# Kernel tuning notes

Hardware: AMD Instinct MI355X
Metric: run time of the kernel (lower is better)

## Reference

```python
import jax, jax.numpy as jnp
import numpy as np

B, S, D = 32, 576, 768
G = 24  # sqrt(S)
TEMP = 0.01


def grid_sample_bilinear_zeros(img, grid):
    # img: (B,C,H,W), grid: (B,Hg,Wg,2) in [-1,1]; torch F.grid_sample,
    # mode='bilinear', padding_mode='zeros', align_corners=False
    Bn, C, H, W = img.shape
    gx, gy = grid[..., 0], grid[..., 1]
    ix = ((gx + 1.0) * W - 1.0) * 0.5
    iy = ((gy + 1.0) * H - 1.0) * 0.5
    x0 = jnp.floor(ix); y0 = jnp.floor(iy)
    x1 = x0 + 1.0;      y1 = y0 + 1.0
    wx1 = ix - x0; wx0 = 1.0 - wx1
    wy1 = iy - y0; wy0 = 1.0 - wy1

    def gather(xi, yi):
        valid = (xi >= 0) & (xi <= W - 1) & (yi >= 0) & (yi <= H - 1)
        xc = jnp.clip(xi, 0, W - 1).astype(jnp.int32)
        yc = jnp.clip(yi, 0, H - 1).astype(jnp.int32)
        vals = jax.vmap(lambda im, y, x: im[:, y, x])(img, yc, xc)  # (B,C,Hg,Wg)
        return vals * valid.astype(img.dtype)[:, None, :, :]

    return (gather(x0, y0) * (wx0 * wy0)[:, None]
            + gather(x1, y0) * (wx1 * wy0)[:, None]
            + gather(x0, y1) * (wx0 * wy1)[:, None]
            + gather(x1, y1) * (wx1 * wy1)[:, None])


def key_finder_net(h, W1, b1, W2, b2, W3, b3):
    # fc1 -> relu -> fc2 -> relu -> fc3 -> tanh
    h = jax.nn.relu(h @ W1 + b1)
    h = jax.nn.relu(h @ W2 + b2)
    return jnp.tanh(h @ W3 + b3)


def setup_inputs() -> dict:
    key = jax.random.key(0)
    ks = jax.random.split(key, 16)
    sd = 1.0 / np.sqrt(D)
    inp = {
        'x': jax.random.normal(ks[0], (B, S, D), dtype=jnp.float32),
        'indices': jax.random.randint(ks[1], (B, S), 0, S),
        'Wq': jax.random.normal(ks[2], (D, D), dtype=jnp.float32) * sd,
        'bq': jnp.zeros((D,), jnp.float32),
        'Wk': jax.random.normal(ks[3], (D, D), dtype=jnp.float32) * sd,
        'bk': jnp.zeros((D,), jnp.float32),
        'Wv': jax.random.normal(ks[4], (D, D), dtype=jnp.float32) * sd,
        'bv': jnp.zeros((D,), jnp.float32),
        'W1': jax.random.normal(ks[5], (2 * D, 60), dtype=jnp.float32) / np.sqrt(2 * D),
        'b1': jnp.zeros((60,), jnp.float32),
        'W2': jax.random.normal(ks[6], (60, 60), dtype=jnp.float32) / np.sqrt(60),
        'b2': jnp.zeros((60,), jnp.float32),
        'W3': jax.random.normal(ks[7], (60, 2), dtype=jnp.float32) / np.sqrt(60),
        'b3': jnp.zeros((2,), jnp.float32),
    }
    return inp


def reference(x, indices, Wq, bq, Wk, bk, Wv, bv, W1, b1, W2, b2, W3, b3):
    q = x @ Wq + bq  # (B,S,D)
    k = x @ Wk + bk
    v = x @ Wv + bv

    sample = key_finder_net(jnp.concatenate([q, k], axis=2), W1, b1, W2, b2, W3, b3)  # (B,S,2)
    # torch: cat((sample_x, sample_y), dim=1).reshape(B,G,G,2)
    flat = jnp.concatenate([sample[:, :, 0], sample[:, :, 1]], axis=1)  # (B,2S)
    grid = flat.reshape(B, G, G, 2)

    k_img = jnp.transpose(k, (0, 2, 1)).reshape(B, D, G, G)
    v_img = jnp.transpose(v, (0, 2, 1)).reshape(B, D, G, G)

    sk = grid_sample_bilinear_zeros(k_img, grid)  # (B,D,G,G)
    sv = grid_sample_bilinear_zeros(v_img, grid)
    sampled_key = jnp.transpose(sk.reshape(B, D, G * G), (0, 2, 1))   # (B,S,D)
    sampled_value = jnp.transpose(sv.reshape(B, D, G * G), (0, 2, 1))

    scores = jnp.sum(q * sampled_key, axis=-1)  # (B,S)
    return jax.nn.sigmoid(TEMP * scores)[..., None] * sampled_value
```

## Files before the change

kernel.cpp:

```cpp
#include <hip/hip_runtime.h>

typedef _Float16 f16;
typedef _Float16 f16x8 __attribute__((ext_vector_type(8)));
typedef _Float16 f16x4 __attribute__((ext_vector_type(4)));
typedef float f32x4 __attribute__((ext_vector_type(4)));

constexpr int NB = 32, NS = 576, ND = 768, NG = 24;
constexpr int M_TOT = NB * NS;
constexpr int N_TOT = 3 * ND;

__global__ void cast_x_kernel(const float* __restrict__ x, f16* __restrict__ xb) {
  int i = (blockIdx.x * 256 + threadIdx.x) * 4;
  float4 v = *(const float4*)(x + i);
  f16x4 o;
  o.x = (f16)v.x; o.y = (f16)v.y; o.z = (f16)v.z; o.w = (f16)v.w;
  *(f16x4*)(xb + i) = o;
}

__global__ void cast_w_kernel(const float* __restrict__ Wq, const float* __restrict__ Wk,
                              const float* __restrict__ Wv, f16* __restrict__ WT) {
  int t = blockIdx.x * 256 + threadIdx.x;
  int n = t / ND, k = t % ND;
  const float* src = (n >= 2 * ND) ? Wv : ((n >= ND) ? Wk : Wq);
  int nn = (n >= 2 * ND) ? n - 2 * ND : ((n >= ND) ? n - ND : n);
  WT[t] = (f16)src[k * ND + nn];
}

__global__ void wcT_kernel(const float* __restrict__ Wq, const float* __restrict__ Wk,
                           const float* __restrict__ bq, const float* __restrict__ bk,
                           const float* __restrict__ W1, const float* __restrict__ b1,
                           f16* __restrict__ WcT_hi, f16* __restrict__ WcT_lo,
                           float* __restrict__ bc) {
  if (blockIdx.x == 192) {
    int c = threadIdx.x;
    if (c < 60) {
      float acc = b1[c];
      for (int j = 0; j < ND; j++)
        acc += bq[j] * W1[j * 60 + c] + bk[j] * W1[(ND + j) * 60 + c];
      bc[c] = acc;
    }
    return;
  }
  int flat = blockIdx.x * 256 + threadIdx.x;
  int r = flat >> 6, c = flat & 63;
  float acc = 0.f;
  if (c < 60) {
    const float* wq = Wq + (size_t)r * ND;
    const float* wk = Wk + (size_t)r * ND;
    for (int j = 0; j < ND; j++)
      acc += wq[j] * W1[j * 60 + c] + wk[j] * W1[(ND + j) * 60 + c];
  }
  f16 hi = (f16)acc;
  f16 lo = (f16)(acc - (float)hi);
  WcT_hi[(size_t)c * ND + r] = hi;
  WcT_lo[(size_t)c * ND + r] = lo;
}

__device__ __forceinline__ void async_copy16(const f16* g, f16* l) {
  __builtin_amdgcn_global_load_lds((const __attribute__((address_space(1))) void*)g,
                                   (__attribute__((address_space(3))) void*)l, 16, 0, 0);
}

__global__ __launch_bounds__(256) void gemm_kernel(const f16* __restrict__ A,
                                                   const f16* __restrict__ Bt,
                                                   const float* __restrict__ bq,
                                                   const float* __restrict__ bk,
                                                   const float* __restrict__ bv,
                                                   f16* __restrict__ C) {
  constexpr int BM = 128, BN = 128, BK = 32;
  __shared__ __align__(16) f16 sA[BM * BK];
  __shared__ __align__(16) f16 sB[BN * BK];

  int bm = blockIdx.x % (M_TOT / BM);
  int bn = blockIdx.x / (M_TOT / BM);
  int tid = threadIdx.x;
  int wave = tid >> 6, lane = tid & 63;
  int wm = (wave >> 1) * 64, wn = (wave & 1) * 64;
  int m0 = bm * BM, n0 = bn * BN;

  int srow = tid >> 2;
  int skc = (tid & 3) * 8;

  f32x4 acc[4][4];
#pragma unroll
  for (int i = 0; i < 4; i++)
#pragma unroll
    for (int j = 0; j < 4; j++) acc[i][j] = 0.f;

  int q = lane >> 4, r16 = lane & 15;

  for (int kk = 0; kk < ND; kk += BK) {
    async_copy16(A + (size_t)(m0 + srow) * ND + kk + skc, sA + tid * 8);
    async_copy16(A + (size_t)(m0 + 64 + srow) * ND + kk + skc, sA + 2048 + tid * 8);
    async_copy16(Bt + (size_t)(n0 + srow) * ND + kk + skc, sB + tid * 8);
    async_copy16(Bt + (size_t)(n0 + 64 + srow) * ND + kk + skc, sB + 2048 + tid * 8);
    __syncthreads();

    f16x8 aF[4], bF[4];
#pragma unroll
    for (int mt = 0; mt < 4; mt++)
      aF[mt] = *(const f16x8*)(sA + (wm + mt * 16 + r16) * BK + q * 8);
#pragma unroll
    for (int nt = 0; nt < 4; nt++)
      bF[nt] = *(const f16x8*)(sB + (wn + nt * 16 + r16) * BK + q * 8);
#pragma unroll
    for (int mt = 0; mt < 4; mt++)
#pragma unroll
      for (int nt = 0; nt < 4; nt++)
        acc[mt][nt] = __builtin_amdgcn_mfma_f32_16x16x32_f16(aF[mt], bF[nt], acc[mt][nt], 0, 0, 0);
    __syncthreads();
  }

#pragma unroll
  for (int nt = 0; nt < 4; nt++) {
    int gn = n0 + wn + nt * 16 + r16;
    float bias = (gn < ND) ? bq[gn] : ((gn < 2 * ND) ? bk[gn - ND] : bv[gn - 2 * ND]);
#pragma unroll
    for (int mt = 0; mt < 4; mt++) {
#pragma unroll
      for (int r = 0; r < 4; r++) {
        int gm = m0 + wm + mt * 16 + q * 4 + r;
        C[(size_t)gm * N_TOT + gn] = (f16)(acc[mt][nt][r] + bias);
      }
    }
  }
}

__global__ __launch_bounds__(256) void z1_mfma_kernel(const float* __restrict__ x,
                                                      const f16* __restrict__ WcT_hi,
                                                      const f16* __restrict__ WcT_lo,
                                                      const float* __restrict__ bc,
                                                      float* __restrict__ h1) {
  int wave = threadIdx.x >> 6, lane = threadIdx.x & 63;
  int q = lane >> 4, r16 = lane & 15;
  int m0 = blockIdx.x * 64 + wave * 16;
  const float* xr = x + (size_t)(m0 + r16) * ND;

  f32x4 acc[4];
#pragma unroll
  for (int nf = 0; nf < 4; nf++) acc[nf] = 0.f;

  for (int kk = 0; kk < ND; kk += 32) {
    int ko = kk + q * 8;
    float4 v0 = *(const float4*)(xr + ko);
    float4 v1 = *(const float4*)(xr + ko + 4);
    f16x8 a_hi, a_lo;
    float xv[8] = {v0.x, v0.y, v0.z, v0.w, v1.x, v1.y, v1.z, v1.w};
#pragma unroll
    for (int j = 0; j < 8; j++) {
      f16 h = (f16)xv[j];
      a_hi[j] = h;
      a_lo[j] = (f16)(xv[j] - (float)h);
    }
    f16x8 b_hi[4], b_lo[4];
#pragma unroll
    for (int nf = 0; nf < 4; nf++) {
      size_t off = (size_t)(nf * 16 + r16) * ND + ko;
      b_hi[nf] = *(const f16x8*)(WcT_hi + off);
      b_lo[nf] = *(const f16x8*)(WcT_lo + off);
    }
#pragma unroll
    for (int nf = 0; nf < 4; nf++) {
      acc[nf] = __builtin_amdgcn_mfma_f32_16x16x32_f16(a_hi, b_hi[nf], acc[nf], 0, 0, 0);
      acc[nf] = __builtin_amdgcn_mfma_f32_16x16x32_f16(a_lo, b_hi[nf], acc[nf], 0, 0, 0);
      acc[nf] = __builtin_amdgcn_mfma_f32_16x16x32_f16(a_hi, b_lo[nf], acc[nf], 0, 0, 0);
    }
  }

#pragma unroll
  for (int nf = 0; nf < 4; nf++) {
    int col = nf * 16 + r16;
    if (col < 60) {
      float bcv = bc[col];
#pragma unroll
      for (int r = 0; r < 4; r++)
        h1[(size_t)(m0 + q * 4 + r) * 60 + col] = fmaxf(acc[nf][r] + bcv, 0.f);
    }
  }
}

__global__ void mlp_tail_kernel(const float* __restrict__ h1, const float* __restrict__ W2,
                                const float* __restrict__ b2, const float* __restrict__ W3,
                                const float* __restrict__ b3, float* __restrict__ coords) {
  int m = (blockIdx.x * 256 + threadIdx.x) >> 6;
  int lane = threadIdx.x & 63;
  int cl = (lane < 60) ? lane : 59;
  const float* h = h1 + (size_t)m * 60;
  float acc = b2[cl];
  for (int j = 0; j < 60; j++) acc = fmaf(h[j], W2[j * 60 + cl], acc);
  float h2 = fmaxf(acc, 0.f);
  float p0 = (lane < 60) ? h2 * W3[cl * 2 + 0] : 0.f;
  float p1 = (lane < 60) ? h2 * W3[cl * 2 + 1] : 0.f;
#pragma unroll
  for (int o = 32; o > 0; o >>= 1) { p0 += __shfl_down(p0, o); p1 += __shfl_down(p1, o); }
  if (lane == 0) {
    float s0 = tanhf(p0 + b3[0]);
    float s1 = tanhf(p1 + b3[1]);
    int b = m / NS, s = m % NS;
    float* cb = coords + (size_t)b * (2 * NS);
    cb[(s >> 1) * 2 + (s & 1)] = s0;
    cb[(288 + (s >> 1)) * 2 + (s & 1)] = s1;
  }
}

__global__ __launch_bounds__(256) void sample_kernel(const f16* __restrict__ qkv,
                                                     const float* __restrict__ coords,
                                                     float* __restrict__ out) {
  int blk = blockIdx.x;
  int b = blk / NS, p = blk % NS;
  int tid = threadIdx.x;

  float gx = coords[(size_t)b * (2 * NS) + p * 2 + 0];
  float gy = coords[(size_t)b * (2 * NS) + p * 2 + 1];
  float ix = ((gx + 1.f) * (float)NG - 1.f) * 0.5f;
  float iy = ((gy + 1.f) * (float)NG - 1.f) * 0.5f;
  float x0f = floorf(ix), y0f = floorf(iy);
  float wx1 = ix - x0f, wx0 = 1.f - wx1;
  float wy1 = iy - y0f, wy0 = 1.f - wy1;
  int x0 = (int)x0f, y0 = (int)y0f, x1 = x0 + 1, y1 = y0 + 1;
  bool vx0 = (x0 >= 0) & (x0 <= NG - 1), vx1 = (x1 >= 0) & (x1 <= NG - 1);
  bool vy0 = (y0 >= 0) & (y0 <= NG - 1), vy1 = (y1 >= 0) & (y1 <= NG - 1);
  int cx0 = min(max(x0, 0), NG - 1), cx1 = min(max(x1, 0), NG - 1);
  int cy0 = min(max(y0, 0), NG - 1), cy1 = min(max(y1, 0), NG - 1);
  float w00 = wx0 * wy0 * ((vx0 && vy0) ? 1.f : 0.f);
  float w10 = wx1 * wy0 * ((vx1 && vy0) ? 1.f : 0.f);
  float w01 = wx0 * wy1 * ((vx0 && vy1) ? 1.f : 0.f);
  float w11 = wx1 * wy1 * ((vx1 && vy1) ? 1.f : 0.f);

  size_t base = (size_t)b * NS;
  const f16* r00 = qkv + (base + cy0 * NG + cx0) * N_TOT;
  const f16* r10 = qkv + (base + cy0 * NG + cx1) * N_TOT;
  const f16* r01 = qkv + (base + cy1 * NG + cx0) * N_TOT;
  const f16* r11 = qkv + (base + cy1 * NG + cx1) * N_TOT;
  const f16* qr  = qkv + (base + p) * N_TOT;

  float partial = 0.f;
  float svs[3];
#pragma unroll
  for (int i = 0; i < 3; i++) {
    int d = tid + i * 256;
    float sk = w00 * (float)r00[ND + d] + w10 * (float)r10[ND + d]
             + w01 * (float)r01[ND + d] + w11 * (float)r11[ND + d];
    float sv = w00 * (float)r00[2 * ND + d] + w10 * (float)r10[2 * ND + d]
             + w01 * (float)r01[2 * ND + d] + w11 * (float)r11[2 * ND + d];
    partial = fmaf((float)qr[d], sk, partial);
    svs[i] = sv;
  }
  __shared__ float red[4];
#pragma unroll
  for (int o = 32; o > 0; o >>= 1) partial += __shfl_down(partial, o);
  if ((tid & 63) == 0) red[tid >> 6] = partial;
  __syncthreads();
  float score = red[0] + red[1] + red[2] + red[3];
  float sig = 1.f / (1.f + expf(-0.01f * score));
  float* orow = out + (size_t)(base + p) * ND;
#pragma unroll
  for (int i = 0; i < 3; i++) orow[tid + i * 256] = sig * svs[i];
}

extern "C" void kernel_launch(void* const* d_in, const int* in_sizes, int n_in,
                              void* d_out, int out_size, void* d_ws, size_t ws_size,
                              hipStream_t stream) {
  const float* x  = (const float*)d_in[0];
  const float* Wq = (const float*)d_in[2];
  const float* bq = (const float*)d_in[3];
  const float* Wk = (const float*)d_in[4];
  const float* bk = (const float*)d_in[5];
  const float* Wv = (const float*)d_in[6];
  const float* bv = (const float*)d_in[7];
  const float* W1 = (const float*)d_in[8];
  const float* b1 = (const float*)d_in[9];
  const float* W2 = (const float*)d_in[10];
  const float* b2 = (const float*)d_in[11];
  const float* W3 = (const float*)d_in[12];
  const float* b3 = (const float*)d_in[13];
  float* out = (float*)d_out;

  char* ws = (char*)d_ws;
  f16*   xb     = (f16*)(ws);
  f16*   WT     = (f16*)(ws + 28311552);
  f16*   qkv    = (f16*)(ws + 31850496);
  f16*   WcT_hi = (f16*)(ws);
  f16*   WcT_lo = (f16*)(ws + 98304);
  float* bc     = (float*)(ws + 116969472);
  float* h1     = (float*)(ws + 116969728);
  float* coords = (float*)(ws + 121393408);

  cast_x_kernel<<<dim3(M_TOT * ND / 1024), dim3(256), 0, stream>>>(x, xb);
  cast_w_kernel<<<dim3(N_TOT * ND / 256), dim3(256), 0, stream>>>(Wq, Wk, Wv, WT);
  gemm_kernel<<<dim3((M_TOT / 128) * (N_TOT / 128)), dim3(256), 0, stream>>>(xb, WT, bq, bk, bv, qkv);
  wcT_kernel<<<dim3(193), dim3(256), 0, stream>>>(Wq, Wk, bq, bk, W1, b1, WcT_hi, WcT_lo, bc);
  z1_mfma_kernel<<<dim3(M_TOT / 64), dim3(256), 0, stream>>>(x, WcT_hi, WcT_lo, bc, h1);
  mlp_tail_kernel<<<dim3(M_TOT / 4), dim3(256), 0, stream>>>(h1, W2, b2, W3, b3, coords);
  sample_kernel<<<dim3(M_TOT), dim3(256), 0, stream>>>(qkv, coords, out);
  (void)in_sizes; (void)n_in; (void)out_size; (void)ws_size;
}
```

Baseline: 411.3 us.

## Fuse x cast into z1, transpose W via LDS, split Wc reduction, vectorize sampler

The standalone x-to-f16 cast is removed; the z1 kernel now writes the f16 high part of x as a side output for the QKV GEMM, so x is read from HBM once. The weight cast-transpose goes through a 64x64 shared-memory tile so both reads and writes are coalesced. The Wq/Wk·W1 precompute is split along K across 8× more blocks with atomic accumulation into a zeroed fp32 buffer, followed by a separate hi/lo split pass. The sampler uses one wave per output row with f16x4 loads and float4 stores, so no LDS reduction or barrier is needed. The trade-offs are extra launches and a memset, plus atomic accumulation order that is not deterministic.

New measurement: 417.7 us. Within noise of the previous version (+1.6%).

```diff
diff --git a/kernel.cpp b/kernel.cpp
--- a/kernel.cpp
+++ b/kernel.cpp
@@ -9,28 +9,50 @@
 constexpr int M_TOT = NB * NS;
 constexpr int N_TOT = 3 * ND;
 
-__global__ void cast_x_kernel(const float* __restrict__ x, f16* __restrict__ xb) {
-  int i = (blockIdx.x * 256 + threadIdx.x) * 4;
-  float4 v = *(const float4*)(x + i);
-  f16x4 o;
-  o.x = (f16)v.x; o.y = (f16)v.y; o.z = (f16)v.z; o.w = (f16)v.w;
-  *(f16x4*)(xb + i) = o;
-}
-
-__global__ void cast_w_kernel(const float* __restrict__ Wq, const float* __restrict__ Wk,
-                              const float* __restrict__ Wv, f16* __restrict__ WT) {
-  int t = blockIdx.x * 256 + threadIdx.x;
-  int n = t / ND, k = t % ND;
-  const float* src = (n >= 2 * ND) ? Wv : ((n >= ND) ? Wk : Wq);
-  int nn = (n >= 2 * ND) ? n - 2 * ND : ((n >= ND) ? n - ND : n);
-  WT[t] = (f16)src[k * ND + nn];
-}
-
-__global__ void wcT_kernel(const float* __restrict__ Wq, const float* __restrict__ Wk,
-                           const float* __restrict__ bq, const float* __restrict__ bk,
-                           const float* __restrict__ W1, const float* __restrict__ b1,
-                           f16* __restrict__ WcT_hi, f16* __restrict__ WcT_lo,
-                           float* __restrict__ bc) {
+__global__ __launch_bounds__(256) void cast_w_t_kernel(const float* __restrict__ Wq,
+                                                       const float* __restrict__ Wk,
+                                                       const float* __restrict__ Wv,
+                                                       f16* __restrict__ WT) {
+  __shared__ float tile[64][65];
+  int bt = blockIdx.x;
+  int ntile = bt / 12, ktile = bt % 12;
+  const float* src = (ntile < 12) ? Wq : ((ntile < 24) ? Wk : Wv);
+  int n0 = (ntile % 12) * 64, k0 = ktile * 64;
+  int cc = threadIdx.x & 63, rr = threadIdx.x >> 6;
+#pragma unroll
+  for (int i = 0; i < 16; i++) {
+    int k = rr + i * 4;
+    tile[cc][k] = src[(size_t)(k0 + k) * ND + n0 + cc];
+  }
+  __syncthreads();
+#pragma unroll
+  for (int i = 0; i < 16; i++) {
+    int n = rr + i * 4;
+    WT[(size_t)(ntile * 64 + n) * ND + k0 + cc] = (f16)tile[n][cc];
+  }
+}
+
+__global__ void wc_partial_kernel(const float* __restrict__ Wq, const float* __restrict__ Wk,
+                                  const float* __restrict__ W1, float* __restrict__ WcfT) {
+  int b = blockIdx.x;
+  int rb = b % 192, jc = b / 192;
+  int flat = rb * 256 + threadIdx.x;
+  int r = flat >> 6, c = flat & 63;
+  if (c >= 60) return;
+  const float* wq = Wq + (size_t)r * ND;
+  const float* wk = Wk + (size_t)r * ND;
+  float acc = 0.f;
+  int j0 = jc * 96;
+  for (int j = j0; j < j0 + 96; j++)
+    acc += wq[j] * W1[j * 60 + c] + wk[j] * W1[(ND + j) * 60 + c];
+  atomicAdd(&WcfT[(size_t)c * ND + r], acc);
+}
+
+__global__ void wc_split_kernel(const float* __restrict__ WcfT,
+                                const float* __restrict__ bq, const float* __restrict__ bk,
+                                const float* __restrict__ W1, const float* __restrict__ b1,
+                                f16* __restrict__ WcT_hi, f16* __restrict__ WcT_lo,
+                                float* __restrict__ bc) {
   if (blockIdx.x == 192) {
     int c = threadIdx.x;
     if (c < 60) {
@@ -41,19 +63,11 @@
     }
     return;
   }
-  int flat = blockIdx.x * 256 + threadIdx.x;
-  int r = flat >> 6, c = flat & 63;
-  float acc = 0.f;
-  if (c < 60) {
-    const float* wq = Wq + (size_t)r * ND;
-    const float* wk = Wk + (size_t)r * ND;
-    for (int j = 0; j < ND; j++)
-      acc += wq[j] * W1[j * 60 + c] + wk[j] * W1[(ND + j) * 60 + c];
-  }
-  f16 hi = (f16)acc;
-  f16 lo = (f16)(acc - (float)hi);
-  WcT_hi[(size_t)c * ND + r] = hi;
-  WcT_lo[(size_t)c * ND + r] = lo;
+  int t = blockIdx.x * 256 + threadIdx.x;
+  float v = WcfT[t];
+  f16 h = (f16)v;
+  WcT_hi[t] = h;
+  WcT_lo[t] = (f16)(v - (float)h);
 }
 
 __device__ __forceinline__ void async_copy16(const f16* g, f16* l) {
@@ -67,16 +81,16 @@
                                                    const float* __restrict__ bk,
                                                    const float* __restrict__ bv,
                                                    f16* __restrict__ C) {
-  constexpr int BM = 128, BN = 128, BK = 32;
+  constexpr int BM = 128, BK = 32;
   __shared__ __align__(16) f16 sA[BM * BK];
-  __shared__ __align__(16) f16 sB[BN * BK];
+  __shared__ __align__(16) f16 sB[BM * BK];
 
   int bm = blockIdx.x % (M_TOT / BM);
   int bn = blockIdx.x / (M_TOT / BM);
   int tid = threadIdx.x;
   int wave = tid >> 6, lane = tid & 63;
   int wm = (wave >> 1) * 64, wn = (wave & 1) * 64;
-  int m0 = bm * BM, n0 = bn * BN;
+  int m0 = bm * BM, n0 = bn * BM;
 
   int srow = tid >> 2;
   int skc = (tid & 3) * 8;
@@ -130,7 +144,8 @@
                                                       const f16* __restrict__ WcT_hi,
                                                       const f16* __restrict__ WcT_lo,
                                                       const float* __restrict__ bc,
-                                                      float* __restrict__ h1) {
+                                                      float* __restrict__ h1,
+                                                      f16* __restrict__ xb) {
   int wave = threadIdx.x >> 6, lane = threadIdx.x & 63;
   int q = lane >> 4, r16 = lane & 15;
   int m0 = blockIdx.x * 64 + wave * 16;
@@ -152,6 +167,7 @@
       a_hi[j] = h;
       a_lo[j] = (f16)(xv[j] - (float)h);
     }
+    *(f16x8*)(xb + (size_t)(m0 + r16) * ND + ko) = a_hi;
     f16x8 b_hi[4], b_lo[4];
 #pragma unroll
     for (int nf = 0; nf < 4; nf++) {
@@ -203,12 +219,12 @@
   }
 }
 
-__global__ __launch_bounds__(256) void sample_kernel(const f16* __restrict__ qkv,
-                                                     const float* __restrict__ coords,
-                                                     float* __restrict__ out) {
+__global__ __launch_bounds__(64) void sample_kernel(const f16* __restrict__ qkv,
+                                                    const float* __restrict__ coords,
+                                                    float* __restrict__ out) {
   int blk = blockIdx.x;
   int b = blk / NS, p = blk % NS;
-  int tid = threadIdx.x;
+  int t = threadIdx.x;
 
   float gx = coords[(size_t)b * (2 * NS) + p * 2 + 0];
   float gy = coords[(size_t)b * (2 * NS) + p * 2 + 1];
@@ -234,28 +250,43 @@
   const f16* r11 = qkv + (base + cy1 * NG + cx1) * N_TOT;
   const f16* qr  = qkv + (base + p) * N_TOT;
 
+  int d0 = t * 12;
   float partial = 0.f;
-  float svs[3];
-#pragma unroll
-  for (int i = 0; i < 3; i++) {
-    int d = tid + i * 256;
-    float sk = w00 * (float)r00[ND + d] + w10 * (float)r10[ND + d]
-             + w01 * (float)r01[ND + d] + w11 * (float)r11[ND + d];
-    float sv = w00 * (float)r00[2 * ND + d] + w10 * (float)r10[2 * ND + d]
-             + w01 * (float)r01[2 * ND + d] + w11 * (float)r11[2 * ND + d];
-    partial = fmaf((float)qr[d], sk, partial);
-    svs[i] = sv;
-  }
-  __shared__ float red[4];
+  float outv[12];
+#pragma unroll
+  for (int ch = 0; ch < 3; ch++) {
+    int d = d0 + ch * 4;
+    f16x4 k00 = *(const f16x4*)(r00 + ND + d);
+    f16x4 k10 = *(const f16x4*)(r10 + ND + d);
+    f16x4 k01 = *(const f16x4*)(r01 + ND + d);
+    f16x4 k11 = *(const f16x4*)(r11 + ND + d);
+    f16x4 v00 = *(const f16x4*)(r00 + 2 * ND + d);
+    f16x4 v10 = *(const f16x4*)(r10 + 2 * ND + d);
+    f16x4 v01 = *(const f16x4*)(r01 + 2 * ND + d);
+    f16x4 v11 = *(const f16x4*)(r11 + 2 * ND + d);
+    f16x4 qv  = *(const f16x4*)(qr + d);
+#pragma unroll
+    for (int j = 0; j < 4; j++) {
+      float sk = w00 * (float)k00[j] + w10 * (float)k10[j]
+               + w01 * (float)k01[j] + w11 * (float)k11[j];
+      float sv = w00 * (float)v00[j] + w10 * (float)v10[j]
+               + w01 * (float)v01[j] + w11 * (float)v11[j];
+      partial = fmaf((float)qv[j], sk, partial);
+      outv[ch * 4 + j] = sv;
+    }
+  }
 #pragma unroll
   for (int o = 32; o > 0; o >>= 1) partial += __shfl_down(partial, o);
-  if ((tid & 63) == 0) red[tid >> 6] = partial;
-  __syncthreads();
-  float score = red[0] + red[1] + red[2] + red[3];
+  float score = __shfl(partial, 0);
   float sig = 1.f / (1.f + expf(-0.01f * score));
   float* orow = out + (size_t)(base + p) * ND;
 #pragma unroll
-  for (int i = 0; i < 3; i++) orow[tid + i * 256] = sig * svs[i];
+  for (int ch = 0; ch < 3; ch++) {
+    float4 st;
+    st.x = sig * outv[ch * 4 + 0]; st.y = sig * outv[ch * 4 + 1];
+    st.z = sig * outv[ch * 4 + 2]; st.w = sig * outv[ch * 4 + 3];
+    *(float4*)(orow + d0 + ch * 4) = st;
+  }
 }
 
 extern "C" void kernel_launch(void* const* d_in, const int* in_sizes, int n_in,
@@ -280,18 +311,20 @@
   f16*   xb     = (f16*)(ws);
   f16*   WT     = (f16*)(ws + 28311552);
   f16*   qkv    = (f16*)(ws + 31850496);
-  f16*   WcT_hi = (f16*)(ws);
-  f16*   WcT_lo = (f16*)(ws + 98304);
+  f16*   WcT_hi = (f16*)(ws + 31850496);
+  f16*   WcT_lo = (f16*)(ws + 31948800);
+  float* WcfT   = (float*)(ws + 32047104);
   float* bc     = (float*)(ws + 116969472);
   float* h1     = (float*)(ws + 116969728);
   float* coords = (float*)(ws + 121393408);
 
-  cast_x_kernel<<<dim3(M_TOT * ND / 1024), dim3(256), 0, stream>>>(x, xb);
-  cast_w_kernel<<<dim3(N_TOT * ND / 256), dim3(256), 0, stream>>>(Wq, Wk, Wv, WT);
+  cast_w_t_kernel<<<dim3(432), dim3(256), 0, stream>>>(Wq, Wk, Wv, WT);
+  hipMemsetAsync(WcfT, 0, 64 * ND * sizeof(float), stream);
+  wc_partial_kernel<<<dim3(1536), dim3(256), 0, stream>>>(Wq, Wk, W1, WcfT);
+  wc_split_kernel<<<dim3(193), dim3(256), 0, stream>>>(WcfT, bq, bk, W1, b1, WcT_hi, WcT_lo, bc);
+  z1_mfma_kernel<<<dim3(M_TOT / 64), dim3(256), 0, stream>>>(x, WcT_hi, WcT_lo, bc, h1, xb);
   gemm_kernel<<<dim3((M_TOT / 128) * (N_TOT / 128)), dim3(256), 0, stream>>>(xb, WT, bq, bk, bv, qkv);
-  wcT_kernel<<<dim3(193), dim3(256), 0, stream>>>(Wq, Wk, bq, bk, W1, b1, WcT_hi, WcT_lo, bc);
-  z1_mfma_kernel<<<dim3(M_TOT / 64), dim3(256), 0, stream>>>(x, WcT_hi, WcT_lo, bc, h1);
   mlp_tail_kernel<<<dim3(M_TOT / 4), dim3(256), 0, stream>>>(h1, W2, b2, W3, b3, coords);
-  sample_kernel<<<dim3(M_TOT), dim3(256), 0, stream>>>(qkv, coords, out);
+  sample_kernel<<<dim3(M_TOT), dim3(64), 0, stream>>>(qkv, coords, out);
   (void)in_sizes; (void)n_in; (void)out_size; (void)ws_size;
 }
```
